# Kernel optimization log

Hardware: AMD Instinct MI355X
Metric: run time of the kernel (lower is better)

The kernel has to match this reference:

```python
import jax, jax.numpy as jnp
import numpy as np

B, L, D, KD, H = 4, 2048, 512, 64, 8


def _dequant(w_int, scale, zp):
    # per-tensor asymmetric dequantization: (q - zero_point) * scale
    return (w_int.astype(jnp.float32) - zp) * scale


def setup_inputs() -> dict:
    key = jax.random.key(0)
    ks = jax.random.split(key, 20)
    inp = {
        'query': jax.random.normal(ks[0], (B, L, D), jnp.float32),
        'key':   jax.random.normal(ks[1], (B, L, D), jnp.float32),
        'value': jax.random.normal(ks[2], (B, L, D), jnp.float32),
        'wq_q': jax.random.randint(ks[3], (D, KD, H), 0, 127, jnp.int32),
        'wk_q': jax.random.randint(ks[4], (D, KD, H), 0, 127, jnp.int32),
        'wv_q': jax.random.randint(ks[5], (D, KD, H), 0, 127, jnp.int32),
        'wo_q': jax.random.randint(ks[6], (KD * H, D), 0, 127, jnp.int32),
        'bq': jax.random.normal(ks[7], (KD, H), jnp.float32) * 0.02,
        'bk': jax.random.normal(ks[8], (KD, H), jnp.float32) * 0.02,
        'bv': jax.random.normal(ks[9], (KD, H), jnp.float32) * 0.02,
        'bo': jax.random.normal(ks[10], (D,), jnp.float32) * 0.02,
        'scale_q': jax.random.uniform(ks[11], (), jnp.float32, 0.001, 0.01),
        'scale_k': jax.random.uniform(ks[12], (), jnp.float32, 0.001, 0.01),
        'scale_v': jax.random.uniform(ks[13], (), jnp.float32, 0.001, 0.01),
        'scale_o': jax.random.uniform(ks[14], (), jnp.float32, 0.001, 0.01),
        'zp_q': jax.random.uniform(ks[15], (), jnp.float32, 50.0, 70.0),
        'zp_k': jax.random.uniform(ks[16], (), jnp.float32, 50.0, 70.0),
        'zp_v': jax.random.uniform(ks[17], (), jnp.float32, 50.0, 70.0),
        'zp_o': jax.random.uniform(ks[18], (), jnp.float32, 50.0, 70.0),
    }
    return inp


def reference(query, key, value, wq_q, wk_q, wv_q, wo_q, bq, bk, bv, bo,
              scale_q, scale_k, scale_v, scale_o, zp_q, zp_k, zp_v, zp_o):
    # Dequantize int8 weights (quantized-inference path of the layer)
    wq = _dequant(wq_q, scale_q, zp_q)  # (D, KD, H)
    wk = _dequant(wk_q, scale_k, zp_k)
    wv = _dequant(wv_q, scale_v, zp_v)
    wo = _dequant(wo_q, scale_o, zp_o)  # (KD*H, D)

    q = jnp.einsum('bij,jkh->bikh', query, wq) + bq  # (B, L, KD, H)
    k = jnp.einsum('bij,jkh->bikh', key,   wk) + bk
    v = jnp.einsum('bij,jkh->bikh', value, wv) + bv

    # scores: contract over key_dim -> (B, Lq, Lk, H)
    scores = jnp.einsum('bidh,bjdh->bijh', q, k) / jnp.sqrt(jnp.float32(KD))
    # tf softmax over axis=-2 of bikh == key axis (axis 2 here)
    attn = jax.nn.softmax(scores, axis=2)
    out = jnp.einsum('bijh,bjdh->bidh', attn, v)  # (B, L, KD, H)
    out = out.reshape(out.shape[0], out.shape[1], KD * H)  # flatten (d,h) row-major, same as tf.reshape
    return jnp.matmul(out, wo) + bo
```

## Files before the change

kernel.cpp:

```cpp
#include <hip/hip_runtime.h>
#include <math.h>
#include <stdint.h>

#define BB 4
#define LL 2048
#define DD 512
#define KDIM 64
#define HH 8

typedef _Float16 f16;
typedef f16 f16x8 __attribute__((ext_vector_type(8)));
typedef f16 f16x4v __attribute__((ext_vector_type(4)));
typedef float f32x4 __attribute__((ext_vector_type(4)));

__device__ __forceinline__ int swz(int x) { return x ^ (((x >> 7) & 7) << 4); }

__device__ __forceinline__ void gload16(const void* g, void* l) {
    __builtin_amdgcn_global_load_lds(
        (const __attribute__((address_space(1))) void*)g,
        (__attribute__((address_space(3))) void*)l, 16, 0, 0);
}

__device__ __forceinline__ void wait_barrier() {
    asm volatile("s_waitcnt vmcnt(0)" ::: "memory");
    __builtin_amdgcn_s_barrier();
}

__global__ __launch_bounds__(256)
void prologue(const int* __restrict__ w0, const int* __restrict__ w1,
              const int* __restrict__ w2, const int* __restrict__ w3,
              const float* s0, const float* s1, const float* s2, const float* s3,
              const float* z0, const float* z1, const float* z2, const float* z3,
              f16* o0, f16* o1, f16* o2, f16* o3,
              const float* __restrict__ xq, const float* __restrict__ xk,
              const float* __restrict__ xv, f16* cq, f16* ck, f16* cv)
{
    __shared__ float t[32][33];
    const int bid = blockIdx.x;
    if (bid < 1024) {
        const int zi = bid >> 8, rem = bid & 255;
        const int* W = zi == 0 ? w0 : zi == 1 ? w1 : zi == 2 ? w2 : w3;
        const float sc = *(zi == 0 ? s0 : zi == 1 ? s1 : zi == 2 ? s2 : s3);
        const float zp = *(zi == 0 ? z0 : zi == 1 ? z1 : zi == 2 ? z2 : z3);
        f16* WT = zi == 0 ? o0 : zi == 1 ? o1 : zi == 2 ? o2 : o3;
        const int n0 = (rem & 15) * 32, k0 = (rem >> 4) * 32;
        const int x = threadIdx.x & 31, y = threadIdx.x >> 5;
        #pragma unroll
        for (int i = 0; i < 32; i += 8)
            t[y + i][x] = ((float)W[(size_t)(k0 + y + i) * DD + n0 + x] - zp) * sc;
        __syncthreads();
        if (zi == 3) {
            const int k = k0 + x;
            const int kp = (k & 7) * 64 + (k >> 3);
            #pragma unroll
            for (int i = 0; i < 32; i += 8)
                WT[(size_t)(n0 + y + i) * DD + kp] = (f16)t[x][y + i];
        } else {
            #pragma unroll
            for (int i = 0; i < 32; i += 8)
                WT[(size_t)(n0 + y + i) * DD + k0 + x] = (f16)t[x][y + i];
        }
    } else {
        const int c = bid - 1024;
        const int yi = c >> 12, xb = c & 4095;
        const float* in = yi == 0 ? xq : yi == 1 ? xk : xv;
        f16* out = yi == 0 ? cq : yi == 1 ? ck : cv;
        const int i = (xb * 256 + threadIdx.x) * 4;
        float4 v = *(const float4*)(in + i);
        f16x4v o = {(f16)v.x, (f16)v.y, (f16)v.z, (f16)v.w};
        *(f16x4v*)(out + i) = o;
    }
}

template<int EPI>
__device__ __forceinline__
void gemm_body(char* As, char* Bs, const f16* __restrict__ A,
               const f16* __restrict__ BT, const float* __restrict__ bias,
               void* __restrict__ OutP)
{
    const int tid = threadIdx.x, lane = tid & 63, wid = tid >> 6;
    const int g = lane >> 4, ql = lane & 15;
    const int wm = wid >> 1, wn = wid & 1;
    const int bid = blockIdx.x;
    const int sb = (bid & 7) * 32 + (bid >> 3);
    const int rowBase = (sb >> 2) * 128, colBase = (sb & 3) * 128;

    auto stage = [&](int p, int buf) {
        const int kt = p * 32;
        #pragma unroll
        for (int i = 0; i < 2; ++i) {
            const int xl = i * 4096 + wid * 1024 + lane * 16;
            const int xs = swz(xl);
            const int r = xs >> 6, cb = xs & 63;
            const char* asrc;
            if (EPI == 1) {
                const int m = rowBase + r, b = m >> 11, qq = m & 2047;
                const int kp = kt * 2 + cb;
                asrc = (const char*)A +
                       (((size_t)((b * 8 + (kp >> 7)) * 2048 + qq)) << 7) + (kp & 127);
            } else {
                asrc = (const char*)(A + (size_t)(rowBase + r) * DD + kt) + cb;
            }
            gload16(asrc, As + buf * 8192 + xl);
            gload16((const char*)(BT + (size_t)(colBase + r) * DD + kt) + cb,
                    Bs + buf * 8192 + xl);
        }
    };

    const f32x4 zero = {0.f, 0.f, 0.f, 0.f};
    f32x4 acc[4][4];
    #pragma unroll
    for (int i = 0; i < 4; ++i)
        #pragma unroll
        for (int j = 0; j < 4; ++j) acc[i][j] = zero;

    stage(0, 0);

    for (int p = 0; p < 16; ++p) {
        const int buf = p & 1;
        wait_barrier();
        if (p < 15) stage(p + 1, buf ^ 1);
        const char* as = As + buf * 8192;
        const char* bs = Bs + buf * 8192;
        f16x8 af[4], bf[4];
        #pragma unroll
        for (int mf = 0; mf < 4; ++mf)
            af[mf] = *(const f16x8*)(as + swz((wm * 64 + mf * 16 + ql) * 64 + g * 16));
        #pragma unroll
        for (int nf = 0; nf < 4; ++nf)
            bf[nf] = *(const f16x8*)(bs + swz((wn * 64 + nf * 16 + ql) * 64 + g * 16));
        __builtin_amdgcn_s_setprio(1);
        #pragma unroll
        for (int mf = 0; mf < 4; ++mf)
            #pragma unroll
            for (int nf = 0; nf < 4; ++nf)
                acc[mf][nf] = __builtin_amdgcn_mfma_f32_16x16x32_f16(af[mf], bf[nf], acc[mf][nf], 0, 0, 0);
        __builtin_amdgcn_s_setprio(0);
    }

    #pragma unroll
    for (int nf = 0; nf < 4; ++nf) {
        const int n = colBase + wn * 64 + nf * 16 + ql;
        const float bn = bias[n];
        #pragma unroll
        for (int mf = 0; mf < 4; ++mf) {
            const int m0 = rowBase + wm * 64 + mf * 16 + g * 4;
            if (EPI == 2) {
                const int b = m0 >> 11, l0 = m0 & 2047;
                const int kd = n >> 3, hh = n & 7;
                f16x4v o = {(f16)(acc[mf][nf][0] + bn), (f16)(acc[mf][nf][1] + bn),
                            (f16)(acc[mf][nf][2] + bn), (f16)(acc[mf][nf][3] + bn)};
                *(f16x4v*)((f16*)OutP + ((size_t)(b * HH + hh) * KDIM + kd) * LL + l0) = o;
            } else {
                #pragma unroll
                for (int r = 0; r < 4; ++r) {
                    const int m = m0 + r;
                    const float v = acc[mf][nf][r] + bn;
                    if (EPI == 0) {
                        const int b = m >> 11, lr = m & 2047;
                        const int kd = n >> 3, hh = n & 7;
                        ((f16*)OutP)[((size_t)(b * HH + hh) * LL + lr) * KDIM + kd] = (f16)v;
                    } else {
                        ((float*)OutP)[(size_t)m * DD + n] = v;
                    }
                }
            }
        }
    }
}

__global__ __launch_bounds__(256)
void gemm_qkv(const f16* Xq, const f16* Xk, const f16* Xv,
              const f16* WTq, const f16* WTk, const f16* WTv,
              const float* bq, const float* bk, const float* bv,
              f16* Qh, f16* Kh, f16* VhT)
{
    __shared__ __align__(16) char As[2 * 128 * 32 * 2];
    __shared__ __align__(16) char Bs[2 * 128 * 32 * 2];
    const int z = blockIdx.z;
    if (z == 0)      gemm_body<0>(As, Bs, Xq, WTq, bq, Qh);
    else if (z == 1) gemm_body<0>(As, Bs, Xk, WTk, bk, Kh);
    else             gemm_body<2>(As, Bs, Xv, WTv, bv, VhT);
}

__global__ __launch_bounds__(256)
void gemm_out(const f16* A, const f16* BT, const float* bias, float* Out)
{
    __shared__ __align__(16) char As[2 * 128 * 32 * 2];
    __shared__ __align__(16) char Bs[2 * 128 * 32 * 2];
    gemm_body<1>(As, Bs, A, BT, bias, Out);
}

__global__ __launch_bounds__(128, 4)
void attn_f16(const f16* __restrict__ Qh, const f16* __restrict__ Kh,
              const f16* __restrict__ VhT, f16* __restrict__ Ob)
{
    __shared__ __align__(16) char k_s[64 * 128];
    __shared__ __align__(16) char v_s[64 * 128];
    __shared__ __align__(16) char p_s[2 * 2048];

    const int tid = threadIdx.x, lane = tid & 63, wid = tid >> 6;
    const int g = lane >> 4, ql = lane & 15;
    char* pw = p_s + wid * 2048;

    const int bid = blockIdx.x;
    const int sb = (bid & 7) * 256 + (bid >> 3);
    const int qt = sb & 63, bh = sb >> 6;

    const f16*  Qb = Qh + (size_t)bh * LL * KDIM;
    const char* Kb = (const char*)(Kh + (size_t)bh * LL * KDIM);
    const char* Vb = (const char*)(VhT + (size_t)bh * KDIM * LL);
    const int q0 = qt * 32 + wid * 16;

    auto stage = [&](int t) {
        const int kv = t * 64;
        #pragma unroll
        for (int i = 0; i < 4; ++i) {
            const int xl = i * 2048 + wid * 1024 + lane * 16;
            const int xs = swz(xl);
            gload16(Kb + (size_t)kv * 128 + xs, k_s + xl);
            gload16(Vb + (size_t)(xs >> 7) * (LL * 2) + (size_t)kv * 2 + (xs & 127),
                    v_s + xl);
        }
    };

    const f16 qscale = (f16)(0.125f * 1.44269504089f);
    f16x8 qfr[2];
    #pragma unroll
    for (int kb = 0; kb < 2; ++kb) {
        qfr[kb] = *(const f16x8*)(Qb + (size_t)(q0 + ql) * KDIM + kb * 32 + g * 8);
        qfr[kb] *= qscale;
    }

    const f32x4 zero = {0.f, 0.f, 0.f, 0.f};
    f32x4 acc[4];
    #pragma unroll
    for (int n = 0; n < 4; ++n) acc[n] = zero;
    float m_r = -1e30f, l_r = 0.f;

    for (int t = 0; t < 32; ++t) {
        stage(t);
        __syncthreads();

        f32x4 s[4];
        __builtin_amdgcn_s_setprio(1);
        #pragma unroll
        for (int kf = 0; kf < 4; ++kf) {
            f16x8 kfr0 = *(const f16x8*)(k_s + swz((kf * 16 + ql) * 128 + g * 16));
            f16x8 kfr1 = *(const f16x8*)(k_s + swz((kf * 16 + ql) * 128 + 64 + g * 16));
            f32x4 z = zero;
            z = __builtin_amdgcn_mfma_f32_16x16x32_f16(kfr0, qfr[0], z, 0, 0, 0);
            z = __builtin_amdgcn_mfma_f32_16x16x32_f16(kfr1, qfr[1], z, 0, 0, 0);
            s[kf] = z;
        }
        __builtin_amdgcn_s_setprio(0);

        float a0 = fmaxf(fmaxf(s[0][0], s[0][1]), s[0][2]);
        float a1 = fmaxf(fmaxf(s[0][3], s[1][0]), s[1][1]);
        float a2 = fmaxf(fmaxf(s[1][2], s[1][3]), s[2][0]);
        float a3 = fmaxf(fmaxf(s[2][1], s[2][2]), s[2][3]);
        float a4 = fmaxf(fmaxf(s[3][0], s[3][1]), s[3][2]);
        float mx = fmaxf(fmaxf(fmaxf(a0, a1), fmaxf(a2, a3)),
                         fmaxf(a4, s[3][3]));
        mx = fmaxf(mx, __shfl_xor(mx, 16));
        mx = fmaxf(mx, __shfl_xor(mx, 32));
        if (__any(mx > m_r + 8.f)) {
            const float mnew = fmaxf(m_r, mx);
            const float fsc = exp2f(m_r - mnew);
            m_r = mnew;
            l_r *= fsc;
            #pragma unroll
            for (int n = 0; n < 4; ++n) acc[n] *= fsc;
        }
        float ps = 0.f;
        #pragma unroll
        for (int kf = 0; kf < 4; ++kf) {
            const float p0 = exp2f(s[kf][0] - m_r);
            const float p1 = exp2f(s[kf][1] - m_r);
            const float p2 = exp2f(s[kf][2] - m_r);
            const float p3 = exp2f(s[kf][3] - m_r);
            ps += (p0 + p1) + (p2 + p3);
            f16x4v pk = {(f16)p0, (f16)p1, (f16)p2, (f16)p3};
            *(f16x4v*)(pw + swz(ql * 128 + kf * 32 + g * 8)) = pk;
        }
        l_r += ps;

        __builtin_amdgcn_s_setprio(1);
        #pragma unroll
        for (int kb = 0; kb < 2; ++kb) {
            f16x8 pf = *(const f16x8*)(pw + swz(ql * 128 + kb * 64 + g * 16));
            #pragma unroll
            for (int n = 0; n < 4; ++n) {
                f16x8 vf = *(const f16x8*)(v_s + swz((n * 16 + ql) * 128
                                                     + kb * 64 + g * 16));
                acc[n] = __builtin_amdgcn_mfma_f32_16x16x32_f16(vf, pf, acc[n], 0, 0, 0);
            }
        }
        __builtin_amdgcn_s_setprio(0);
        __syncthreads();
    }

    l_r += __shfl_xor(l_r, 16);
    l_r += __shfl_xor(l_r, 32);
    const float inv = 1.f / l_r;
    const int q = q0 + ql;
    f16* orow = Ob + ((size_t)bh * LL + q) * KDIM;
    #pragma unroll
    for (int n = 0; n < 4; ++n) {
        f16x4v o = {(f16)(acc[n][0] * inv), (f16)(acc[n][1] * inv),
                    (f16)(acc[n][2] * inv), (f16)(acc[n][3] * inv)};
        *(f16x4v*)(orow + n * 16 + g * 4) = o;
    }
}

extern "C" void kernel_launch(void* const* d_in, const int* in_sizes, int n_in,
                              void* d_out, int out_size, void* d_ws, size_t ws_size,
                              hipStream_t stream)
{
    const float* query = (const float*)d_in[0];
    const float* key   = (const float*)d_in[1];
    const float* value = (const float*)d_in[2];
    const int* wq = (const int*)d_in[3];
    const int* wk = (const int*)d_in[4];
    const int* wv = (const int*)d_in[5];
    const int* wo = (const int*)d_in[6];
    const float* bq = (const float*)d_in[7];
    const float* bk = (const float*)d_in[8];
    const float* bv = (const float*)d_in[9];
    const float* bo = (const float*)d_in[10];
    const float* scale_q = (const float*)d_in[11];
    const float* scale_k = (const float*)d_in[12];
    const float* scale_v = (const float*)d_in[13];
    const float* scale_o = (const float*)d_in[14];
    const float* zp_q = (const float*)d_in[15];
    const float* zp_k = (const float*)d_in[16];
    const float* zp_v = (const float*)d_in[17];
    const float* zp_o = (const float*)d_in[18];

    const size_t MD = (size_t)BB * LL * DD;
    const size_t WT_SZ = (size_t)DD * DD;

    f16* Xq  = (f16*)d_ws;
    f16* Xk  = Xq + MD;
    f16* Xv  = Xk + MD;
    f16* WTq = Xv + MD;
    f16* WTk = WTq + WT_SZ;
    f16* WTv = WTk + WT_SZ;
    f16* WTo = WTv + WT_SZ;
    f16* Qh  = WTo + WT_SZ;
    f16* Kh  = Qh + MD;
    f16* VhT = Kh + MD;
    f16* Ob  = VhT + MD;

    prologue<<<1024 + 3 * 4096, 256, 0, stream>>>(
        wq, wk, wv, wo, scale_q, scale_k, scale_v, scale_o,
        zp_q, zp_k, zp_v, zp_o, WTq, WTk, WTv, WTo,
        query, key, value, Xq, Xk, Xv);

    dim3 gg(256, 1, 3);
    gemm_qkv<<<gg, 256, 0, stream>>>(Xq, Xk, Xv, WTq, WTk, WTv,
                                     bq, bk, bv, Qh, Kh, VhT);

    attn_f16<<<2048, 128, 0, stream>>>(Qh, Kh, VhT, Ob);

    gemm_out<<<256, 256, 0, stream>>>(Ob, WTo, bo, (float*)d_out);
}
```

Measured before the change: 157.0 us.

## Process two 16-row query tiles per wave to reuse K/V fragments

Each wave in the attention kernel now handles 32 query rows (two 16-row tiles) instead of 16, so a block covers 64 queries and the grid is halved. K fragments are loaded from LDS once and used for both tiles' QK^T MFMAs, and each V fragment feeds two PV MFMAs. This also halves the global K/V staging traffic per query. In exchange it doubles the per-wave accumulators and P scratch, raising register and LDS use, and leaves fewer blocks to fill the GPU.

```diff
diff --git a/kernel.cpp b/kernel.cpp
--- a/kernel.cpp
+++ b/kernel.cpp
@@ -197,20 +197,20 @@
 {
     __shared__ __align__(16) char k_s[64 * 128];
     __shared__ __align__(16) char v_s[64 * 128];
-    __shared__ __align__(16) char p_s[2 * 2048];
+    __shared__ __align__(16) char p_s[2 * 4096];
 
     const int tid = threadIdx.x, lane = tid & 63, wid = tid >> 6;
     const int g = lane >> 4, ql = lane & 15;
-    char* pw = p_s + wid * 2048;
+    char* pw = p_s + wid * 4096;
 
     const int bid = blockIdx.x;
-    const int sb = (bid & 7) * 256 + (bid >> 3);
-    const int qt = sb & 63, bh = sb >> 6;
+    const int sb = (bid & 7) * 128 + (bid >> 3);
+    const int qt = sb & 31, bh = sb >> 5;
 
     const f16*  Qb = Qh + (size_t)bh * LL * KDIM;
     const char* Kb = (const char*)(Kh + (size_t)bh * LL * KDIM);
     const char* Vb = (const char*)(VhT + (size_t)bh * KDIM * LL);
-    const int q0 = qt * 32 + wid * 16;
+    const int q0 = qt * 64 + wid * 32;
 
     auto stage = [&](int t) {
         const int kv = t * 64;
@@ -225,91 +225,115 @@
     };
 
     const f16 qscale = (f16)(0.125f * 1.44269504089f);
-    f16x8 qfr[2];
-    #pragma unroll
-    for (int kb = 0; kb < 2; ++kb) {
-        qfr[kb] = *(const f16x8*)(Qb + (size_t)(q0 + ql) * KDIM + kb * 32 + g * 8);
-        qfr[kb] *= qscale;
-    }
+    f16x8 qfr[2][2];
+    #pragma unroll
+    for (int i2 = 0; i2 < 2; ++i2)
+        #pragma unroll
+        for (int kb = 0; kb < 2; ++kb) {
+            qfr[i2][kb] = *(const f16x8*)(Qb + (size_t)(q0 + i2 * 16 + ql) * KDIM
+                                          + kb * 32 + g * 8);
+            qfr[i2][kb] *= qscale;
+        }
 
     const f32x4 zero = {0.f, 0.f, 0.f, 0.f};
-    f32x4 acc[4];
-    #pragma unroll
-    for (int n = 0; n < 4; ++n) acc[n] = zero;
-    float m_r = -1e30f, l_r = 0.f;
+    f32x4 acc[2][4];
+    float m_r[2], l_r[2];
+    #pragma unroll
+    for (int i2 = 0; i2 < 2; ++i2) {
+        m_r[i2] = -1e30f; l_r[i2] = 0.f;
+        #pragma unroll
+        for (int n = 0; n < 4; ++n) acc[i2][n] = zero;
+    }
 
     for (int t = 0; t < 32; ++t) {
         stage(t);
         __syncthreads();
 
-        f32x4 s[4];
+        f16x8 kfr[4][2];
+        #pragma unroll
+        for (int kf = 0; kf < 4; ++kf) {
+            kfr[kf][0] = *(const f16x8*)(k_s + swz((kf * 16 + ql) * 128 + g * 16));
+            kfr[kf][1] = *(const f16x8*)(k_s + swz((kf * 16 + ql) * 128 + 64 + g * 16));
+        }
+
+        #pragma unroll
+        for (int i2 = 0; i2 < 2; ++i2) {
+            f32x4 s[4];
+            __builtin_amdgcn_s_setprio(1);
+            #pragma unroll
+            for (int kf = 0; kf < 4; ++kf) {
+                f32x4 z = zero;
+                z = __builtin_amdgcn_mfma_f32_16x16x32_f16(kfr[kf][0], qfr[i2][0], z, 0, 0, 0);
+                z = __builtin_amdgcn_mfma_f32_16x16x32_f16(kfr[kf][1], qfr[i2][1], z, 0, 0, 0);
+                s[kf] = z;
+            }
+            __builtin_amdgcn_s_setprio(0);
+
+            float a0 = fmaxf(fmaxf(s[0][0], s[0][1]), s[0][2]);
+            float a1 = fmaxf(fmaxf(s[0][3], s[1][0]), s[1][1]);
+            float a2 = fmaxf(fmaxf(s[1][2], s[1][3]), s[2][0]);
+            float a3 = fmaxf(fmaxf(s[2][1], s[2][2]), s[2][3]);
+            float a4 = fmaxf(fmaxf(s[3][0], s[3][1]), s[3][2]);
+            float mx = fmaxf(fmaxf(fmaxf(a0, a1), fmaxf(a2, a3)),
+                             fmaxf(a4, s[3][3]));
+            mx = fmaxf(mx, __shfl_xor(mx, 16));
+            mx = fmaxf(mx, __shfl_xor(mx, 32));
+            if (__any(mx > m_r[i2] + 8.f)) {
+                const float mnew = fmaxf(m_r[i2], mx);
+                const float fsc = exp2f(m_r[i2] - mnew);
+                m_r[i2] = mnew;
+                l_r[i2] *= fsc;
+                #pragma unroll
+                for (int n = 0; n < 4; ++n) acc[i2][n] *= fsc;
+            }
+            float ps = 0.f;
+            #pragma unroll
+            for (int kf = 0; kf < 4; ++kf) {
+                const float p0 = exp2f(s[kf][0] - m_r[i2]);
+                const float p1 = exp2f(s[kf][1] - m_r[i2]);
+                const float p2 = exp2f(s[kf][2] - m_r[i2]);
+                const float p3 = exp2f(s[kf][3] - m_r[i2]);
+                ps += (p0 + p1) + (p2 + p3);
+                f16x4v pk = {(f16)p0, (f16)p1, (f16)p2, (f16)p3};
+                *(f16x4v*)(pw + swz((i2 * 16 + ql) * 128 + kf * 32 + g * 8)) = pk;
+            }
+            l_r[i2] += ps;
+        }
+
         __builtin_amdgcn_s_setprio(1);
         #pragma unroll
-        for (int kf = 0; kf < 4; ++kf) {
-            f16x8 kfr0 = *(const f16x8*)(k_s + swz((kf * 16 + ql) * 128 + g * 16));
-            f16x8 kfr1 = *(const f16x8*)(k_s + swz((kf * 16 + ql) * 128 + 64 + g * 16));
-            f32x4 z = zero;
-            z = __builtin_amdgcn_mfma_f32_16x16x32_f16(kfr0, qfr[0], z, 0, 0, 0);
-            z = __builtin_amdgcn_mfma_f32_16x16x32_f16(kfr1, qfr[1], z, 0, 0, 0);
-            s[kf] = z;
-        }
-        __builtin_amdgcn_s_setprio(0);
-
-        float a0 = fmaxf(fmaxf(s[0][0], s[0][1]), s[0][2]);
-        float a1 = fmaxf(fmaxf(s[0][3], s[1][0]), s[1][1]);
-        float a2 = fmaxf(fmaxf(s[1][2], s[1][3]), s[2][0]);
-        float a3 = fmaxf(fmaxf(s[2][1], s[2][2]), s[2][3]);
-        float a4 = fmaxf(fmaxf(s[3][0], s[3][1]), s[3][2]);
-        float mx = fmaxf(fmaxf(fmaxf(a0, a1), fmaxf(a2, a3)),
-                         fmaxf(a4, s[3][3]));
-        mx = fmaxf(mx, __shfl_xor(mx, 16));
-        mx = fmaxf(mx, __shfl_xor(mx, 32));
-        if (__any(mx > m_r + 8.f)) {
-            const float mnew = fmaxf(m_r, mx);
-            const float fsc = exp2f(m_r - mnew);
-            m_r = mnew;
-            l_r *= fsc;
-            #pragma unroll
-            for (int n = 0; n < 4; ++n) acc[n] *= fsc;
-        }
-        float ps = 0.f;
-        #pragma unroll
-        for (int kf = 0; kf < 4; ++kf) {
-            const float p0 = exp2f(s[kf][0] - m_r);
-            const float p1 = exp2f(s[kf][1] - m_r);
-            const float p2 = exp2f(s[kf][2] - m_r);
-            const float p3 = exp2f(s[kf][3] - m_r);
-            ps += (p0 + p1) + (p2 + p3);
-            f16x4v pk = {(f16)p0, (f16)p1, (f16)p2, (f16)p3};
-            *(f16x4v*)(pw + swz(ql * 128 + kf * 32 + g * 8)) = pk;
-        }
-        l_r += ps;
-
-        __builtin_amdgcn_s_setprio(1);
-        #pragma unroll
         for (int kb = 0; kb < 2; ++kb) {
-            f16x8 pf = *(const f16x8*)(pw + swz(ql * 128 + kb * 64 + g * 16));
+            f16x8 pf[2];
+            #pragma unroll
+            for (int i2 = 0; i2 < 2; ++i2)
+                pf[i2] = *(const f16x8*)(pw + swz((i2 * 16 + ql) * 128 + kb * 64 + g * 16));
             #pragma unroll
             for (int n = 0; n < 4; ++n) {
                 f16x8 vf = *(const f16x8*)(v_s + swz((n * 16 + ql) * 128
                                                      + kb * 64 + g * 16));
-                acc[n] = __builtin_amdgcn_mfma_f32_16x16x32_f16(vf, pf, acc[n], 0, 0, 0);
+                #pragma unroll
+                for (int i2 = 0; i2 < 2; ++i2)
+                    acc[i2][n] = __builtin_amdgcn_mfma_f32_16x16x32_f16(vf, pf[i2], acc[i2][n], 0, 0, 0);
             }
         }
         __builtin_amdgcn_s_setprio(0);
         __syncthreads();
     }
 
-    l_r += __shfl_xor(l_r, 16);
-    l_r += __shfl_xor(l_r, 32);
-    const float inv = 1.f / l_r;
-    const int q = q0 + ql;
-    f16* orow = Ob + ((size_t)bh * LL + q) * KDIM;
-    #pragma unroll
-    for (int n = 0; n < 4; ++n) {
-        f16x4v o = {(f16)(acc[n][0] * inv), (f16)(acc[n][1] * inv),
-                    (f16)(acc[n][2] * inv), (f16)(acc[n][3] * inv)};
-        *(f16x4v*)(orow + n * 16 + g * 4) = o;
+    #pragma unroll
+    for (int i2 = 0; i2 < 2; ++i2) {
+        float l = l_r[i2];
+        l += __shfl_xor(l, 16);
+        l += __shfl_xor(l, 32);
+        const float inv = 1.f / l;
+        const int q = q0 + i2 * 16 + ql;
+        f16* orow = Ob + ((size_t)bh * LL + q) * KDIM;
+        #pragma unroll
+        for (int n = 0; n < 4; ++n) {
+            f16x4v o = {(f16)(acc[i2][n][0] * inv), (f16)(acc[i2][n][1] * inv),
+                        (f16)(acc[i2][n][2] * inv), (f16)(acc[i2][n][3] * inv)};
+            *(f16x4v*)(orow + n * 16 + g * 4) = o;
+        }
     }
 }
 
@@ -361,7 +385,7 @@
     gemm_qkv<<<gg, 256, 0, stream>>>(Xq, Xk, Xv, WTq, WTk, WTv,
                                      bq, bk, bv, Qh, Kh, VhT);
 
-    attn_f16<<<2048, 128, 0, stream>>>(Qh, Kh, VhT, Ob);
+    attn_f16<<<1024, 128, 0, stream>>>(Qh, Kh, VhT, Ob);
 
     gemm_out<<<256, 256, 0, stream>>>(Ob, WTo, bo, (float*)d_out);
 }
```

Measured after the change: 154.4 us. About the same (-1.6%).

## Enlarge attention blocks to 8 waves and 128-wide KV tiles

Applied to the files above, without the earlier changes.

The attention kernel now uses 512-thread blocks (8 waves, 128 queries per block) instead of 128-thread blocks, and processes 128 keys per iteration instead of 64. Each K/V tile loaded into LDS is therefore shared by four times as many query rows, with half as many barrier iterations. This cuts global K/V traffic and sync overhead, at the cost of a larger LDS footprint (about 64KB per block) and more registers for the score fragments, which may lower occupancy. The swizzle is split into 128- and 256-byte row variants to match the new LDS layouts.

```diff
diff --git a/kernel.cpp b/kernel.cpp
--- a/kernel.cpp
+++ b/kernel.cpp
@@ -13,7 +13,8 @@
 typedef f16 f16x4v __attribute__((ext_vector_type(4)));
 typedef float f32x4 __attribute__((ext_vector_type(4)));
 
-__device__ __forceinline__ int swz(int x) { return x ^ (((x >> 7) & 7) << 4); }
+__device__ __forceinline__ int swz7(int x) { return x ^ (((x >> 7) & 7) << 4); }
+__device__ __forceinline__ int swz8(int x) { return x ^ (((x >> 8) & 7) << 4); }
 
 __device__ __forceinline__ void gload16(const void* g, void* l) {
     __builtin_amdgcn_global_load_lds(
@@ -90,7 +91,7 @@
         #pragma unroll
         for (int i = 0; i < 2; ++i) {
             const int xl = i * 4096 + wid * 1024 + lane * 16;
-            const int xs = swz(xl);
+            const int xs = swz7(xl);
             const int r = xs >> 6, cb = xs & 63;
             const char* asrc;
             if (EPI == 1) {
@@ -125,10 +126,10 @@
         f16x8 af[4], bf[4];
         #pragma unroll
         for (int mf = 0; mf < 4; ++mf)
-            af[mf] = *(const f16x8*)(as + swz((wm * 64 + mf * 16 + ql) * 64 + g * 16));
+            af[mf] = *(const f16x8*)(as + swz7((wm * 64 + mf * 16 + ql) * 64 + g * 16));
         #pragma unroll
         for (int nf = 0; nf < 4; ++nf)
-            bf[nf] = *(const f16x8*)(bs + swz((wn * 64 + nf * 16 + ql) * 64 + g * 16));
+            bf[nf] = *(const f16x8*)(bs + swz7((wn * 64 + nf * 16 + ql) * 64 + g * 16));
         __builtin_amdgcn_s_setprio(1);
         #pragma unroll
         for (int mf = 0; mf < 4; ++mf)
@@ -191,35 +192,34 @@
     gemm_body<1>(As, Bs, A, BT, bias, Out);
 }
 
-__global__ __launch_bounds__(128, 4)
+__global__ __launch_bounds__(512, 4)
 void attn_f16(const f16* __restrict__ Qh, const f16* __restrict__ Kh,
               const f16* __restrict__ VhT, f16* __restrict__ Ob)
 {
-    __shared__ __align__(16) char k_s[64 * 128];
-    __shared__ __align__(16) char v_s[64 * 128];
-    __shared__ __align__(16) char p_s[2 * 2048];
+    __shared__ __align__(16) char k_s[128 * 128];
+    __shared__ __align__(16) char v_s[64 * 256];
+    __shared__ __align__(16) char p_s[8 * 4096];
 
     const int tid = threadIdx.x, lane = tid & 63, wid = tid >> 6;
     const int g = lane >> 4, ql = lane & 15;
-    char* pw = p_s + wid * 2048;
+    char* pw = p_s + wid * 4096;
 
     const int bid = blockIdx.x;
-    const int sb = (bid & 7) * 256 + (bid >> 3);
-    const int qt = sb & 63, bh = sb >> 6;
+    const int sb = (bid & 7) * 64 + (bid >> 3);
+    const int qt = sb & 15, bh = sb >> 4;
 
     const f16*  Qb = Qh + (size_t)bh * LL * KDIM;
     const char* Kb = (const char*)(Kh + (size_t)bh * LL * KDIM);
     const char* Vb = (const char*)(VhT + (size_t)bh * KDIM * LL);
-    const int q0 = qt * 32 + wid * 16;
+    const int q0 = qt * 128 + wid * 16;
 
     auto stage = [&](int t) {
-        const int kv = t * 64;
-        #pragma unroll
-        for (int i = 0; i < 4; ++i) {
-            const int xl = i * 2048 + wid * 1024 + lane * 16;
-            const int xs = swz(xl);
-            gload16(Kb + (size_t)kv * 128 + xs, k_s + xl);
-            gload16(Vb + (size_t)(xs >> 7) * (LL * 2) + (size_t)kv * 2 + (xs & 127),
+        #pragma unroll
+        for (int i = 0; i < 2; ++i) {
+            const int xl = i * 8192 + wid * 1024 + lane * 16;
+            gload16(Kb + (size_t)t * 16384 + swz7(xl), k_s + xl);
+            const int xv = swz8(xl);
+            gload16(Vb + (size_t)(xl >> 8) * (LL * 2) + t * 256 + (xv & 255),
                     v_s + xl);
         }
     };
@@ -238,16 +238,16 @@
     for (int n = 0; n < 4; ++n) acc[n] = zero;
     float m_r = -1e30f, l_r = 0.f;
 
-    for (int t = 0; t < 32; ++t) {
+    for (int t = 0; t < 16; ++t) {
         stage(t);
         __syncthreads();
 
-        f32x4 s[4];
+        f32x4 s[8];
         __builtin_amdgcn_s_setprio(1);
         #pragma unroll
-        for (int kf = 0; kf < 4; ++kf) {
-            f16x8 kfr0 = *(const f16x8*)(k_s + swz((kf * 16 + ql) * 128 + g * 16));
-            f16x8 kfr1 = *(const f16x8*)(k_s + swz((kf * 16 + ql) * 128 + 64 + g * 16));
+        for (int kf = 0; kf < 8; ++kf) {
+            f16x8 kfr0 = *(const f16x8*)(k_s + swz7((kf * 16 + ql) * 128 + g * 16));
+            f16x8 kfr1 = *(const f16x8*)(k_s + swz7((kf * 16 + ql) * 128 + 64 + g * 16));
             f32x4 z = zero;
             z = __builtin_amdgcn_mfma_f32_16x16x32_f16(kfr0, qfr[0], z, 0, 0, 0);
             z = __builtin_amdgcn_mfma_f32_16x16x32_f16(kfr1, qfr[1], z, 0, 0, 0);
@@ -255,13 +255,12 @@
         }
         __builtin_amdgcn_s_setprio(0);
 
-        float a0 = fmaxf(fmaxf(s[0][0], s[0][1]), s[0][2]);
-        float a1 = fmaxf(fmaxf(s[0][3], s[1][0]), s[1][1]);
-        float a2 = fmaxf(fmaxf(s[1][2], s[1][3]), s[2][0]);
-        float a3 = fmaxf(fmaxf(s[2][1], s[2][2]), s[2][3]);
-        float a4 = fmaxf(fmaxf(s[3][0], s[3][1]), s[3][2]);
-        float mx = fmaxf(fmaxf(fmaxf(a0, a1), fmaxf(a2, a3)),
-                         fmaxf(a4, s[3][3]));
+        float t8[8];
+        #pragma unroll
+        for (int kf = 0; kf < 8; ++kf)
+            t8[kf] = fmaxf(fmaxf(s[kf][0], s[kf][1]), fmaxf(s[kf][2], s[kf][3]));
+        float mx = fmaxf(fmaxf(fmaxf(t8[0], t8[1]), fmaxf(t8[2], t8[3])),
+                         fmaxf(fmaxf(t8[4], t8[5]), fmaxf(t8[6], t8[7])));
         mx = fmaxf(mx, __shfl_xor(mx, 16));
         mx = fmaxf(mx, __shfl_xor(mx, 32));
         if (__any(mx > m_r + 8.f)) {
@@ -274,25 +273,25 @@
         }
         float ps = 0.f;
         #pragma unroll
-        for (int kf = 0; kf < 4; ++kf) {
+        for (int kf = 0; kf < 8; ++kf) {
             const float p0 = exp2f(s[kf][0] - m_r);
             const float p1 = exp2f(s[kf][1] - m_r);
             const float p2 = exp2f(s[kf][2] - m_r);
             const float p3 = exp2f(s[kf][3] - m_r);
             ps += (p0 + p1) + (p2 + p3);
             f16x4v pk = {(f16)p0, (f16)p1, (f16)p2, (f16)p3};
-            *(f16x4v*)(pw + swz(ql * 128 + kf * 32 + g * 8)) = pk;
+            *(f16x4v*)(pw + swz8(ql * 256 + kf * 32 + g * 8)) = pk;
         }
         l_r += ps;
 
         __builtin_amdgcn_s_setprio(1);
         #pragma unroll
-        for (int kb = 0; kb < 2; ++kb) {
-            f16x8 pf = *(const f16x8*)(pw + swz(ql * 128 + kb * 64 + g * 16));
+        for (int kb = 0; kb < 4; ++kb) {
+            f16x8 pf = *(const f16x8*)(pw + swz8(ql * 256 + kb * 64 + g * 16));
             #pragma unroll
             for (int n = 0; n < 4; ++n) {
-                f16x8 vf = *(const f16x8*)(v_s + swz((n * 16 + ql) * 128
-                                                     + kb * 64 + g * 16));
+                f16x8 vf = *(const f16x8*)(v_s + swz8((n * 16 + ql) * 256
+                                                      + kb * 64 + g * 16));
                 acc[n] = __builtin_amdgcn_mfma_f32_16x16x32_f16(vf, pf, acc[n], 0, 0, 0);
             }
         }
@@ -361,7 +360,7 @@
     gemm_qkv<<<gg, 256, 0, stream>>>(Xq, Xk, Xv, WTq, WTk, WTv,
                                      bq, bk, bv, Qh, Kh, VhT);
 
-    attn_f16<<<2048, 128, 0, stream>>>(Qh, Kh, VhT, Ob);
+    attn_f16<<<512, 512, 0, stream>>>(Qh, Kh, VhT, Ob);
 
     gemm_out<<<256, 256, 0, stream>>>(Ob, WTo, bo, (float*)d_out);
 }
```

Measured after the change: 141.3 us. -10.0%, faster.
